# Performance work log

Hardware: AMD Instinct MI355X
Metric: run time of the kernel (lower is better)

The kernel has to match this reference:

```python
import jax, jax.numpy as jnp
import numpy as np

D_MODEL = 256
N_HEAD = 4
HEAD_DIM = D_MODEL // N_HEAD  # 64


def setup_inputs() -> dict:
    key = jax.random.key(0)
    kx, kw, kb = jax.random.split(key, 3)
    x = jax.random.normal(kx, (4, 2048, D_MODEL), dtype=jnp.float32)
    # nn.Linear(256, 768): weight [768, 256], bias [768]
    bound = 1.0 / np.sqrt(D_MODEL)
    W_qkv = jax.random.uniform(kw, (3 * D_MODEL, D_MODEL), dtype=jnp.float32, minval=-bound, maxval=bound)
    b_qkv = jax.random.uniform(kb, (3 * D_MODEL,), dtype=jnp.float32, minval=-bound, maxval=bound)
    return {"x": x, "W_qkv": W_qkv, "b_qkv": b_qkv}


def reference(x, W_qkv, b_qkv):
    B, S, _ = x.shape
    # fused QKV projection: [B, S, 3*D]
    qkv = jnp.einsum("bsd,ed->bse", x, W_qkv) + b_qkv
    q, k, v = jnp.split(qkv, 3, axis=-1)
    # [B, S, D] -> [B, H, S, Dh]
    def to_heads(t):
        return t.reshape(B, S, N_HEAD, HEAD_DIM).transpose(0, 2, 1, 3)
    q, k, v = to_heads(q), to_heads(k), to_heads(v)
    scale = 1.0 / np.sqrt(HEAD_DIM)
    # scores [B, H, S, S]
    scores = jnp.einsum("bhqd,bhkd->bhqk", q, k) * scale
    attn = jax.nn.softmax(scores, axis=-1)
    out = jnp.einsum("bhqk,bhkd->bhqd", attn, v)  # [B, H, S, Dh]
    return out
```

## Files before the change

kernel.cpp:

```cpp
#include <hip/hip_runtime.h>

#define BB 4
#define SS 2048
#define DM 256
#define NH 4
#define DH 64
#define NROW (BB*SS)
#define NE   (3*DM)
#define BH   (BB*NH)
#define HEAD_ELEMS (BH*SS*DH)
#define NQROWS (BH*SS)

typedef _Float16 half_t;
typedef __attribute__((ext_vector_type(8))) _Float16 half8;
typedef __attribute__((ext_vector_type(4))) _Float16 half4;
typedef __attribute__((ext_vector_type(4))) float floatx4;

#define KPAD 72

#define QK_SCALE 0.18033688011112042f
#define EXP2(x) __builtin_amdgcn_exp2f(x)
#define DEFER_THR 8.0f

__global__ __launch_bounds__(256) void prep(const float* __restrict__ x,
                                            const float* __restrict__ W,
                                            half_t* __restrict__ xh,
                                            half_t* __restrict__ xl,
                                            half_t* __restrict__ wh) {
    int gtid = blockIdx.x * 256 + threadIdx.x;
    {
        int i = gtid * 4;
        float4 v = *(const float4*)&x[i];
        half4 h, l;
        h.x = (half_t)v.x; l.x = (half_t)(v.x - (float)h.x);
        h.y = (half_t)v.y; l.y = (half_t)(v.y - (float)h.y);
        h.z = (half_t)v.z; l.z = (half_t)(v.z - (float)h.z);
        h.w = (half_t)v.w; l.w = (half_t)(v.w - (float)h.w);
        *(half4*)&xh[i] = h;
        *(half4*)&xl[i] = l;
    }
    if (gtid < NE * DM / 4) {
        int i = gtid * 4;
        float4 v = *(const float4*)&W[i];
        half4 h;
        h.x = (half_t)v.x; h.y = (half_t)v.y;
        h.z = (half_t)v.z; h.w = (half_t)v.w;
        *(half4*)&wh[i] = h;
    }
}

__global__ __launch_bounds__(256) void qkv_proj(const half_t* __restrict__ xh,
                                                const half_t* __restrict__ xl,
                                                const half_t* __restrict__ whg,
                                                const float* __restrict__ bias,
                                                half_t* __restrict__ qh,
                                                half_t* __restrict__ kh,
                                                half_t* __restrict__ vt) {
    __shared__ __align__(16) half_t Xh[64 * KPAD];
    __shared__ __align__(16) half_t Xl[64 * KPAD];
    __shared__ __align__(16) half_t Wh[64 * KPAD];

    const int rb   = blockIdx.x * 64;
    const int nb   = blockIdx.y * 64;
    const int tid  = threadIdx.x;
    const int wid  = tid >> 6;
    const int lane = tid & 63;
    const int quad = lane >> 4;
    const int col  = lane & 15;

    floatx4 acc[4];
    #pragma unroll
    for (int t = 0; t < 4; ++t) acc[t] = (floatx4){0.f, 0.f, 0.f, 0.f};

    for (int k0 = 0; k0 < DM; k0 += 64) {
        __syncthreads();
        #pragma unroll
        for (int i = 0; i < 2; ++i) {
            int gi = tid + 256 * i;
            int r  = gi >> 3;
            int c8 = (gi & 7) * 8;
            *(half8*)&Xh[r * KPAD + c8] = *(const half8*)&xh[(size_t)(rb + r) * DM + k0 + c8];
            *(half8*)&Xl[r * KPAD + c8] = *(const half8*)&xl[(size_t)(rb + r) * DM + k0 + c8];
            *(half8*)&Wh[r * KPAD + c8] = *(const half8*)&whg[(size_t)(nb + r) * DM + k0 + c8];
        }
        __syncthreads();

        half8 ah0 = *(const half8*)&Xh[(wid * 16 + col) * KPAD + quad * 8];
        half8 ah1 = *(const half8*)&Xh[(wid * 16 + col) * KPAD + 32 + quad * 8];
        half8 al0 = *(const half8*)&Xl[(wid * 16 + col) * KPAD + quad * 8];
        half8 al1 = *(const half8*)&Xl[(wid * 16 + col) * KPAD + 32 + quad * 8];

        #pragma unroll
        for (int t = 0; t < 4; ++t) {
            half8 bh0 = *(const half8*)&Wh[(t * 16 + col) * KPAD + quad * 8];
            half8 bh1 = *(const half8*)&Wh[(t * 16 + col) * KPAD + 32 + quad * 8];
            acc[t] = __builtin_amdgcn_mfma_f32_16x16x32_f16(ah0, bh0, acc[t], 0, 0, 0);
            acc[t] = __builtin_amdgcn_mfma_f32_16x16x32_f16(ah1, bh1, acc[t], 0, 0, 0);
            acc[t] = __builtin_amdgcn_mfma_f32_16x16x32_f16(al0, bh0, acc[t], 0, 0, 0);
            acc[t] = __builtin_amdgcn_mfma_f32_16x16x32_f16(al1, bh1, acc[t], 0, 0, 0);
        }
    }

    const int part = nb >> 8;
    const int mloc = wid * 16 + quad * 4;
    if (part != 2) {
        #pragma unroll
        for (int t = 0; t < 4; ++t) {
            int e    = nb + t * 16 + col;
            float be = bias[e];
            int dm   = e & 255;
            int h    = dm >> 6;
            int dh   = dm & 63;
            #pragma unroll
            for (int r = 0; r < 4; ++r) {
                int row = rb + mloc + r;
                int b   = row >> 11;
                int s   = row & 2047;
                int bh_ = b * NH + h;
                float val = acc[t][r] + be;
                if (part == 0) {
                    qh[((size_t)bh_ * SS + s) * DH + dh] = (half_t)(val * QK_SCALE);
                } else {
                    kh[((size_t)bh_ * SS + s) * DH + dh] = (half_t)val;
                }
            }
        }
    } else {
        __syncthreads();
        #pragma unroll
        for (int t = 0; t < 4; ++t) {
            int e    = nb + t * 16 + col;
            float be = bias[e];
            #pragma unroll
            for (int r = 0; r < 4; ++r)
                Xh[(t * 16 + col) * KPAD + mloc + r] = (half_t)(acc[t][r] + be);
        }
        __syncthreads();
        const int b   = rb >> 11;
        const int s0  = rb & 2047;
        const int h   = (nb >> 6) & 3;
        const int bh_ = b * NH + h;
        #pragma unroll
        for (int i = 0; i < 2; ++i) {
            int idx = tid + 256 * i;
            int rr  = idx >> 3;
            int cc8 = (idx & 7) * 8;
            *(half8*)&vt[((size_t)bh_ * DH + rr) * SS + s0 + cc8] =
                *(const half8*)&Xh[rr * KPAD + cc8];
        }
    }
}

__global__ __launch_bounds__(128, 4) void attn(const half_t* __restrict__ qh,
                                               const half_t* __restrict__ kh,
                                               const half_t* __restrict__ vt,
                                               half_t* __restrict__ pO,
                                               float* __restrict__ mst,
                                               float* __restrict__ lst) {
    __shared__ __align__(16) half_t Ks[64 * KPAD];
    __shared__ __align__(16) half_t Vts[64 * KPAD];

    const int lin  = blockIdx.x + 64 * blockIdx.y + 1024 * blockIdx.z;
    const int xcd  = lin & 7;
    const int j    = lin >> 3;
    const int strm = xcd + 8 * (j >> 6);
    const int q0   = (j & 63) * 32;
    const int bh   = strm & 15;
    const int kz   = strm >> 4;

    const size_t base = (size_t)bh * SS * DH;
    const int tid  = threadIdx.x;
    const int wid  = tid >> 6;
    const int lane = tid & 63;
    const int quad = lane >> 4;
    const int col  = lane & 15;
    const int ktBeg = kz * (SS / 2);
    const int ktEnd = ktBeg + (SS / 2);

    int srr[4], scc[4];
    #pragma unroll
    for (int i = 0; i < 4; ++i) {
        int gi = tid + 128 * i;
        srr[i] = gi >> 3;
        scc[i] = (gi & 7) * 8;
    }

    half8 bq0, bq1;
    {
        int s = q0 + wid * 16 + col;
        bq0 = *(const half8*)&qh[base + (size_t)s * DH + quad * 8];
        bq1 = *(const half8*)&qh[base + (size_t)s * DH + 32 + quad * 8];
    }

    half8 nk[4], nv[4];
    #pragma unroll
    for (int i = 0; i < 4; ++i) {
        nk[i] = *(const half8*)&kh[base + (size_t)(ktBeg + srr[i]) * DH + scc[i]];
        nv[i] = *(const half8*)&vt[base + (size_t)srr[i] * SS + ktBeg + scc[i]];
    }

    float m_i = -3.0e38f;
    float l_part = 0.f;
    floatx4 o[4];
    #pragma unroll
    for (int dt = 0; dt < 4; ++dt) o[dt] = (floatx4){0.f, 0.f, 0.f, 0.f};

    for (int kt = ktBeg; kt < ktEnd; kt += 64) {
        __syncthreads();
        #pragma unroll
        for (int i = 0; i < 4; ++i) {
            *(half8*)&Ks[srr[i] * KPAD + scc[i]]  = nk[i];
            *(half8*)&Vts[srr[i] * KPAD + scc[i]] = nv[i];
        }
        __syncthreads();

        const int ktn = kt + 64;
        if (ktn < ktEnd) {
            #pragma unroll
            for (int i = 0; i < 4; ++i) {
                nk[i] = *(const half8*)&kh[base + (size_t)(ktn + srr[i]) * DH + scc[i]];
                nv[i] = *(const half8*)&vt[base + (size_t)srr[i] * SS + ktn + scc[i]];
            }
        }

        floatx4 sc[4];
        #pragma unroll
        for (int t = 0; t < 4; ++t) {
            half8 ak0 = *(const half8*)&Ks[(t * 16 + col) * KPAD + quad * 8];
            half8 ak1 = *(const half8*)&Ks[(t * 16 + col) * KPAD + 32 + quad * 8];
            floatx4 c = (floatx4){0.f, 0.f, 0.f, 0.f};
            c = __builtin_amdgcn_mfma_f32_16x16x32_f16(ak0, bq0, c, 0, 0, 0);
            c = __builtin_amdgcn_mfma_f32_16x16x32_f16(ak1, bq1, c, 0, 0, 0);
            sc[t] = c;
        }

        float mloc = -3.0e38f;
        #pragma unroll
        for (int t = 0; t < 4; ++t) {
            float a = fmaxf(fmaxf(sc[t][0], sc[t][1]), fmaxf(sc[t][2], sc[t][3]));
            mloc = fmaxf(mloc, a);
        }
        mloc = fmaxf(mloc, __shfl_xor(mloc, 16));
        mloc = fmaxf(mloc, __shfl_xor(mloc, 32));

        bool skip = __all(mloc <= m_i + DEFER_THR);
        float m_new = skip ? m_i : fmaxf(m_i, mloc);

        half4 pa[4];
        float rsumL = 0.f;
        #pragma unroll
        for (int t = 0; t < 4; ++t) {
            float p0 = EXP2(sc[t][0] - m_new);
            float p1 = EXP2(sc[t][1] - m_new);
            float p2 = EXP2(sc[t][2] - m_new);
            float p3 = EXP2(sc[t][3] - m_new);
            rsumL += p0 + p1 + p2 + p3;
            pa[t] = (half4){(half_t)p0, (half_t)p1, (half_t)p2, (half_t)p3};
        }

        if (skip) {
            l_part += rsumL;
        } else {
            float alpha = EXP2(m_i - m_new);
            m_i = m_new;
            l_part = l_part * alpha + rsumL;
            float ar[4];
            #pragma unroll
            for (int i = 0; i < 4; ++i) ar[i] = __shfl(alpha, quad * 4 + i);
            #pragma unroll
            for (int dt = 0; dt < 4; ++dt)
                #pragma unroll
                for (int i = 0; i < 4; ++i)
                    o[dt][i] *= ar[i];
        }

        #pragma unroll
        for (int t = 0; t < 4; ++t) {
            #pragma unroll
            for (int dt = 0; dt < 4; ++dt) {
                half4 bv = *(const half4*)&Vts[(dt * 16 + col) * KPAD + t * 16 + quad * 4];
                o[dt] = __builtin_amdgcn_mfma_f32_16x16x16f16(pa[t], bv, o[dt], 0, 0, 0);
            }
        }
    }

    float l_i = l_part + __shfl_xor(l_part, 16);
    l_i += __shfl_xor(l_i, 32);

    const size_t pbase = (size_t)kz * HEAD_ELEMS + base;
    {
        float inv = 1.0f / l_i;
        float ir[4];
        #pragma unroll
        for (int i = 0; i < 4; ++i) ir[i] = __shfl(inv, quad * 4 + i);
        #pragma unroll
        for (int dt = 0; dt < 4; ++dt)
            #pragma unroll
            for (int i = 0; i < 4; ++i) {
                int row = q0 + wid * 16 + quad * 4 + i;
                pO[pbase + (size_t)row * DH + dt * 16 + col] = (half_t)(o[dt][i] * ir[i]);
            }
        if (quad == 0) {
            int row = q0 + wid * 16 + col;
            int idx = kz * NQROWS + bh * SS + row;
            mst[idx] = m_i;
            lst[idx] = l_i;
        }
    }
}

__global__ __launch_bounds__(256) void merge(const half_t* __restrict__ pO,
                                             const float* __restrict__ mst,
                                             const float* __restrict__ lst,
                                             float* __restrict__ out) {
    int gid = blockIdx.x * 256 + threadIdx.x;
    int row = gid >> 3;
    int dc  = (gid & 7) * 8;
    float m1 = mst[row], m2 = mst[NQROWS + row];
    float l1 = lst[row], l2 = lst[NQROWS + row];
    float M  = fmaxf(m1, m2);
    float w1 = l1 * EXP2(m1 - M);
    float w2 = l2 * EXP2(m2 - M);
    float inv = 1.0f / (w1 + w2);
    float a = w1 * inv, b = w2 * inv;
    half8 o1 = *(const half8*)&pO[(size_t)row * DH + dc];
    half8 o2 = *(const half8*)&pO[(size_t)HEAD_ELEMS + (size_t)row * DH + dc];
    float4 r0, r1;
    r0.x = a * (float)o1[0] + b * (float)o2[0];
    r0.y = a * (float)o1[1] + b * (float)o2[1];
    r0.z = a * (float)o1[2] + b * (float)o2[2];
    r0.w = a * (float)o1[3] + b * (float)o2[3];
    r1.x = a * (float)o1[4] + b * (float)o2[4];
    r1.y = a * (float)o1[5] + b * (float)o2[5];
    r1.z = a * (float)o1[6] + b * (float)o2[6];
    r1.w = a * (float)o1[7] + b * (float)o2[7];
    *(float4*)&out[(size_t)row * DH + dc]     = r0;
    *(float4*)&out[(size_t)row * DH + dc + 4] = r1;
}

extern "C" void kernel_launch(void* const* d_in, const int* in_sizes, int n_in,
                              void* d_out, int out_size, void* d_ws, size_t ws_size,
                              hipStream_t stream) {
    const float* x  = (const float*)d_in[0];
    const float* Wq = (const float*)d_in[1];
    const float* bq = (const float*)d_in[2];
    float* out = (float*)d_out;

    half_t* qh  = (half_t*)d_ws;
    half_t* kh  = qh + (size_t)HEAD_ELEMS;
    half_t* vt  = kh + (size_t)HEAD_ELEMS;
    half_t* xh  = vt + (size_t)HEAD_ELEMS;
    half_t* xl  = xh + (size_t)HEAD_ELEMS;
    half_t* whp = xl + (size_t)HEAD_ELEMS;
    half_t* pO  = xh;
    float*  mst = (float*)((char*)d_ws + 21364736);
    float*  lst = mst + 2 * NQROWS;

    prep<<<2048, 256, 0, stream>>>(x, Wq, xh, xl, whp);
    qkv_proj<<<dim3(NROW / 64, NE / 64), 256, 0, stream>>>(xh, xl, whp, bq, qh, kh, vt);
    attn<<<dim3(SS / 32, BH, 2), 128, 0, stream>>>(qh, kh, vt, pO, mst, lst);
    merge<<<1024, 256, 0, stream>>>(pO, mst, lst, out);
}
```

Before: 123.3 us.

## Split attention keys four ways and use 256-thread blocks over 64 query rows

The attention kernel now splits the key range into four partitions instead of two, and each block has 4 waves covering 64 query rows, so each K/V tile in shared memory is reused by more waves. The merge kernel combines four partial outputs with their max and sum statistics, and the partial buffers move to a separate workspace region. This raises the number of in-flight blocks and cuts per-block key work, at the cost of more partial-output traffic and a heavier merge.

Result: slower. 200.2 us (+62.4%).

```diff
diff --git a/kernel.cpp b/kernel.cpp
--- a/kernel.cpp
+++ b/kernel.cpp
@@ -10,6 +10,7 @@
 #define BH   (BB*NH)
 #define HEAD_ELEMS (BH*SS*DH)
 #define NQROWS (BH*SS)
+#define NKZ 4
 
 typedef _Float16 half_t;
 typedef __attribute__((ext_vector_type(8))) _Float16 half8;
@@ -151,7 +152,7 @@
     }
 }
 
-__global__ __launch_bounds__(128, 4) void attn(const half_t* __restrict__ qh,
+__global__ __launch_bounds__(256, 8) void attn(const half_t* __restrict__ qh,
                                                const half_t* __restrict__ kh,
                                                const half_t* __restrict__ vt,
                                                half_t* __restrict__ pO,
@@ -160,11 +161,11 @@
     __shared__ __align__(16) half_t Ks[64 * KPAD];
     __shared__ __align__(16) half_t Vts[64 * KPAD];
 
-    const int lin  = blockIdx.x + 64 * blockIdx.y + 1024 * blockIdx.z;
+    const int lin  = blockIdx.x + 32 * (blockIdx.y + 16 * blockIdx.z);
     const int xcd  = lin & 7;
     const int j    = lin >> 3;
-    const int strm = xcd + 8 * (j >> 6);
-    const int q0   = (j & 63) * 32;
+    const int strm = xcd + 8 * (j >> 5);
+    const int q0   = (j & 31) * 64;
     const int bh   = strm & 15;
     const int kz   = strm >> 4;
 
@@ -174,13 +175,13 @@
     const int lane = tid & 63;
     const int quad = lane >> 4;
     const int col  = lane & 15;
-    const int ktBeg = kz * (SS / 2);
-    const int ktEnd = ktBeg + (SS / 2);
-
-    int srr[4], scc[4];
-    #pragma unroll
-    for (int i = 0; i < 4; ++i) {
-        int gi = tid + 128 * i;
+    const int ktBeg = kz * (SS / NKZ);
+    const int ktEnd = ktBeg + (SS / NKZ);
+
+    int srr[2], scc[2];
+    #pragma unroll
+    for (int i = 0; i < 2; ++i) {
+        int gi = tid + 256 * i;
         srr[i] = gi >> 3;
         scc[i] = (gi & 7) * 8;
     }
@@ -192,9 +193,9 @@
         bq1 = *(const half8*)&qh[base + (size_t)s * DH + 32 + quad * 8];
     }
 
-    half8 nk[4], nv[4];
-    #pragma unroll
-    for (int i = 0; i < 4; ++i) {
+    half8 nk[2], nv[2];
+    #pragma unroll
+    for (int i = 0; i < 2; ++i) {
         nk[i] = *(const half8*)&kh[base + (size_t)(ktBeg + srr[i]) * DH + scc[i]];
         nv[i] = *(const half8*)&vt[base + (size_t)srr[i] * SS + ktBeg + scc[i]];
     }
@@ -208,7 +209,7 @@
     for (int kt = ktBeg; kt < ktEnd; kt += 64) {
         __syncthreads();
         #pragma unroll
-        for (int i = 0; i < 4; ++i) {
+        for (int i = 0; i < 2; ++i) {
             *(half8*)&Ks[srr[i] * KPAD + scc[i]]  = nk[i];
             *(half8*)&Vts[srr[i] * KPAD + scc[i]] = nv[i];
         }
@@ -217,7 +218,7 @@
         const int ktn = kt + 64;
         if (ktn < ktEnd) {
             #pragma unroll
-            for (int i = 0; i < 4; ++i) {
+            for (int i = 0; i < 2; ++i) {
                 nk[i] = *(const half8*)&kh[base + (size_t)(ktn + srr[i]) * DH + scc[i]];
                 nv[i] = *(const half8*)&vt[base + (size_t)srr[i] * SS + ktn + scc[i]];
             }
@@ -316,24 +317,28 @@
     int gid = blockIdx.x * 256 + threadIdx.x;
     int row = gid >> 3;
     int dc  = (gid & 7) * 8;
-    float m1 = mst[row], m2 = mst[NQROWS + row];
-    float l1 = lst[row], l2 = lst[NQROWS + row];
-    float M  = fmaxf(m1, m2);
-    float w1 = l1 * EXP2(m1 - M);
-    float w2 = l2 * EXP2(m2 - M);
-    float inv = 1.0f / (w1 + w2);
-    float a = w1 * inv, b = w2 * inv;
-    half8 o1 = *(const half8*)&pO[(size_t)row * DH + dc];
-    half8 o2 = *(const half8*)&pO[(size_t)HEAD_ELEMS + (size_t)row * DH + dc];
-    float4 r0, r1;
-    r0.x = a * (float)o1[0] + b * (float)o2[0];
-    r0.y = a * (float)o1[1] + b * (float)o2[1];
-    r0.z = a * (float)o1[2] + b * (float)o2[2];
-    r0.w = a * (float)o1[3] + b * (float)o2[3];
-    r1.x = a * (float)o1[4] + b * (float)o2[4];
-    r1.y = a * (float)o1[5] + b * (float)o2[5];
-    r1.z = a * (float)o1[6] + b * (float)o2[6];
-    r1.w = a * (float)o1[7] + b * (float)o2[7];
+    float m[NKZ], l[NKZ];
+    #pragma unroll
+    for (int p = 0; p < NKZ; ++p) {
+        m[p] = mst[p * NQROWS + row];
+        l[p] = lst[p * NQROWS + row];
+    }
+    float M = fmaxf(fmaxf(m[0], m[1]), fmaxf(m[2], m[3]));
+    float w[NKZ], wsum = 0.f;
+    #pragma unroll
+    for (int p = 0; p < NKZ; ++p) { w[p] = l[p] * EXP2(m[p] - M); wsum += w[p]; }
+    float inv = 1.0f / wsum;
+
+    float r[8] = {0.f,0.f,0.f,0.f,0.f,0.f,0.f,0.f};
+    #pragma unroll
+    for (int p = 0; p < NKZ; ++p) {
+        float a = w[p] * inv;
+        half8 ov = *(const half8*)&pO[(size_t)p * HEAD_ELEMS + (size_t)row * DH + dc];
+        #pragma unroll
+        for (int e = 0; e < 8; ++e) r[e] += a * (float)ov[e];
+    }
+    float4 r0 = {r[0], r[1], r[2], r[3]};
+    float4 r1 = {r[4], r[5], r[6], r[7]};
     *(float4*)&out[(size_t)row * DH + dc]     = r0;
     *(float4*)&out[(size_t)row * DH + dc + 4] = r1;
 }
@@ -352,12 +357,12 @@
     half_t* xh  = vt + (size_t)HEAD_ELEMS;
     half_t* xl  = xh + (size_t)HEAD_ELEMS;
     half_t* whp = xl + (size_t)HEAD_ELEMS;
-    half_t* pO  = xh;
-    float*  mst = (float*)((char*)d_ws + 21364736);
-    float*  lst = mst + 2 * NQROWS;
+    half_t* pO  = (half_t*)d_ws + (size_t)6 * HEAD_ELEMS;
+    float*  mst = (float*)((char*)d_ws + (size_t)10 * HEAD_ELEMS * 2);
+    float*  lst = mst + (size_t)NKZ * NQROWS;
 
     prep<<<2048, 256, 0, stream>>>(x, Wq, xh, xl, whp);
     qkv_proj<<<dim3(NROW / 64, NE / 64), 256, 0, stream>>>(xh, xl, whp, bq, qh, kh, vt);
-    attn<<<dim3(SS / 32, BH, 2), 128, 0, stream>>>(qh, kh, vt, pO, mst, lst);
+    attn<<<dim3(SS / 64, BH, NKZ), 256, 0, stream>>>(qh, kh, vt, pO, mst, lst);
     merge<<<1024, 256, 0, stream>>>(pO, mst, lst, out);
 }
```
